# Optimization experiments

Hardware: AMD Instinct MI355X
Metric: run time of the kernel (lower is better)

Reference implementation:

```python
import jax, jax.numpy as jnp
import numpy as np

B, L, C = 64, 4096, 16
PL, PC, NP, D, FS = 128, 8, 64, 64, 100  # patch_size_L, patch_size_C, num_patches, output_dim, f_s


def setup_inputs() -> dict:
    key = jax.random.key(0)
    ks = jax.random.split(key, 9)
    x = jax.random.normal(ks[0], (B, L, C), dtype=jnp.float32)
    start_L = jax.random.randint(ks[1], (B, NP), 0, L - PL + 1, dtype=jnp.int32)
    idx_C = jax.random.randint(ks[2], (B, NP, PC), 0, C, dtype=jnp.int32)
    W1 = jax.random.normal(ks[3], (2 * PC + 1, D), dtype=jnp.float32) * 0.2
    b1 = jax.random.normal(ks[4], (D,), dtype=jnp.float32) * 0.02
    W2 = jax.random.normal(ks[5], (2 * D + 1, D), dtype=jnp.float32) * 0.1
    b2 = jax.random.normal(ks[6], (D,), dtype=jnp.float32) * 0.02
    W3 = jax.random.normal(ks[7], (PL * D, D), dtype=jnp.float32) * 0.01
    b3 = jax.random.normal(ks[8], (D,), dtype=jnp.float32) * 0.02
    return dict(x=x, start_L=start_L, idx_C=idx_C, W1=W1, b1=b1, W2=W2, b2=b2, W3=W3, b3=b3)


def reference(x, start_L, idx_C, W1, b1, W2, b2, W3, b3):
    T = 1.0 / FS
    # contiguous window indices along L (wrapped), [B, NP, PL]
    idx_L = (start_L[:, :, None] + jnp.arange(PL, dtype=jnp.int32)) % L
    # fused double gather: avoid materializing the [B, NP, L, C] broadcast of the original
    bidx = jnp.arange(B)[:, None, None, None]
    patches = x[bidx, idx_L[:, :, :, None], idx_C[:, :, None, :]]        # [B, NP, PL, PC]
    # time embedding: t = arange(L)*T gathered by idx_L
    t_patches = (idx_L.astype(jnp.float32) * T)[..., None]               # [B, NP, PL, 1]
    # channel embedding: c = arange(C) gathered by idx_C
    c_patches = jnp.broadcast_to(idx_C.astype(jnp.float32)[:, :, None, :], (B, NP, PL, PC))
    feats = jnp.concatenate([patches, t_patches, c_patches], axis=-1)    # [B, NP, PL, 2*PC+1]
    h = jax.nn.silu(feats @ W1 + b1)                                     # [B, NP, PL, D]
    # --- fft branch (computed then discarded by the original module; kept for fidelity) ---
    f = jnp.linspace(0.0, FS / 2.0, PL // 2 + 1)
    fft = jnp.fft.rfft(h, axis=-2, norm='ortho')                         # [B, NP, PL//2+1, D]
    f_patches = jnp.broadcast_to(f[None, None, :, None], (B, NP, PL // 2 + 1, 1))
    fcat = jnp.concatenate([fft.real, fft.imag, f_patches], axis=-1)     # [B, NP, PL//2+1, 2D+1]
    _unused = jax.nn.silu(fcat @ W2 + b2)
    # --- mixer on flattened patches ---
    flat = h.reshape(B, NP, PL * D)                                      # [B, NP, PL*D]
    out = jax.nn.silu(flat @ W3 + b3)                                    # [B, NP, D]
    return out
```

## Files before the change

kernel.cpp:

```cpp
#include <hip/hip_runtime.h>
#include <hip/hip_bf16.h>

#define BB 64
#define LL 4096
#define CC 16
#define PL 128
#define PC 8
#define NPP 64
#define DD 64
#define TSTEP 0.01f

#define KSPLIT 16
#define LT_PER (PL / KSPLIT)
#define NT_MAIN 256
#define NMB BB

#define FRAG_U32 (PL * 8 * 256)
#define SPLIT_STRIDE (NMB * 2 * 2 * 64 * 16)
#define PART_FLT (KSPLIT * SPLIT_STRIDE)

typedef float f32x4  __attribute__((ext_vector_type(4)));
typedef float f32x16 __attribute__((ext_vector_type(16)));
typedef int   i32x4  __attribute__((ext_vector_type(4)));
typedef short s16x8  __attribute__((ext_vector_type(8)));
typedef unsigned int u32;

__device__ __forceinline__ u32 f2bf(float f) {
    u32 u = __float_as_uint(f);
    return (u + 0x7fffu + ((u >> 16) & 1u)) >> 16;
}
__device__ __forceinline__ float silu_f(float z) {
    return z * __builtin_amdgcn_rcpf(1.0f + __expf(-z));
}
__device__ __forceinline__ u32 pk(float lo, float hi) {
    __hip_bfloat162 p = __float22bfloat162_rn(float2{lo, hi});
    u32 r;
    __builtin_memcpy(&r, &p, 4);
    return r;
}
__device__ __forceinline__ s16x8 as8(i32x4 v) {
    s16x8 r;
    __builtin_memcpy(&r, &v, 16);
    return r;
}
__device__ __forceinline__ void plswap(u32& a, u32& b) {
    auto r = __builtin_amdgcn_permlane32_swap(a, b, false, false);
    u32 tmp[2];
    __builtin_memcpy(tmp, &r, 8);
    a = tmp[0]; b = tmp[1];
}

__global__ __launch_bounds__(256) void w3_prep(const float* __restrict__ W3,
                                               u32* __restrict__ wsf) {
    const int tid  = blockIdx.x * 256 + threadIdx.x;
    const int lane = tid & 63;
    const int m    = tid >> 6;
    const int ns   = m & 1;
    const int ksub = (m >> 1) & 1;
    const int kk   = (m >> 2) & 1;
    const int ltg  = m >> 3;
    const int k0   = ltg * 64 + kk * 32 + ksub * 16 + ((lane >> 5) << 3);
    const int col  = (ns << 5) + (lane & 31);
    u32 q[4];
    #pragma unroll
    for (int jj = 0; jj < 4; ++jj)
        q[jj] = pk(W3[(size_t)(k0 + 2 * jj)     * DD + col],
                   W3[(size_t)(k0 + 2 * jj + 1) * DD + col]);
    i32x4 v; v.x = (int)q[0]; v.y = (int)q[1]; v.z = (int)q[2]; v.w = (int)q[3];
    *(i32x4*)(wsf + (size_t)m * 256 + (lane << 2)) = v;
}

__global__ __launch_bounds__(NT_MAIN) void htfe_main(
    const float* __restrict__ x, const int* __restrict__ start_L,
    const int* __restrict__ idx_C, const float* __restrict__ W1,
    const float* __restrict__ b1, const u32* __restrict__ wsf,
    float* __restrict__ part)
{
    __shared__ __align__(16) u32    xqf[LT_PER * 64 * 8];
    __shared__ __align__(16) f32x16 redacc[2][2][64];
    __shared__ int sStart[64];
    __shared__ int sCi[64][PC];

    const int t    = threadIdx.x;
    const int lane = t & 63;
    const int w    = t >> 6;
    const int kk   = w >> 1;
    const int ph   = w & 1;
    const int l31  = lane & 31;
    const bool loH = lane < 32;

    const int mb    = blockIdx.x & (NMB - 1);
    const int split = blockIdx.x >> 6;
    const int b     = mb;
    const int lt0   = split * LT_PER;

    if (t < 64) sStart[t] = start_L[b * NPP + t];
    {
        const int i0 = t, i1 = t + 256;
        sCi[i0 >> 3][i0 & 7] = idx_C[(size_t)b * NPP * PC + i0];
        sCi[i1 >> 3][i1 & 7] = idx_C[(size_t)b * NPP * PC + i1];
    }
    __syncthreads();

    const int p  = ph * 32 + l31;
    const int dA = kk * 32 + l31;
    const float startPf = (float)sStart[p];

    i32x4 a1f0, a1f1;
    if (loH) {
        a1f0.x = (int)pk(W1[0 * DD + dA], W1[1 * DD + dA]);
        a1f0.y = (int)pk(W1[2 * DD + dA], W1[3 * DD + dA]);
        a1f0.z = (int)pk(W1[4 * DD + dA], W1[5 * DD + dA]);
        a1f0.w = (int)pk(W1[6 * DD + dA], W1[7 * DD + dA]);
        a1f1.x = (int)pk(W1[8 * DD + dA], W1[8 * DD + dA]);
        a1f1.y = (int)pk(b1[dA], 0.0f);
        a1f1.z = 0; a1f1.w = 0;
    } else {
        a1f0.x = (int)pk(W1[ 9 * DD + dA], W1[10 * DD + dA]);
        a1f0.y = (int)pk(W1[11 * DD + dA], W1[12 * DD + dA]);
        a1f0.z = (int)pk(W1[13 * DD + dA], W1[14 * DD + dA]);
        a1f0.w = (int)pk(W1[15 * DD + dA], W1[16 * DD + dA]);
        a1f1.x = (int)pk(W1[0 * DD + dA], W1[1 * DD + dA]);
        a1f1.y = (int)pk(W1[2 * DD + dA], W1[3 * DD + dA]);
        a1f1.z = (int)pk(W1[4 * DD + dA], W1[5 * DD + dA]);
        a1f1.w = (int)pk(W1[6 * DD + dA], W1[7 * DD + dA]);
    }
    i32x4 cReg;
    cReg.x = (int)pk((float)sCi[p][0], (float)sCi[p][1]);
    cReg.y = (int)pk((float)sCi[p][2], (float)sCi[p][3]);
    cReg.z = (int)pk((float)sCi[p][4], (float)sCi[p][5]);
    cReg.w = (int)pk((float)sCi[p][6], (float)sCi[p][7]);

    #pragma unroll
    for (int uu = 0; uu < 2; ++uu) {
        const int u  = t * 2 + uu;
        const int lt = u >> 6;
        const int pp = u & 63;
        const float* xrow = x + ((size_t)b * LL + (size_t)(sStart[pp] + lt0 + lt)) * CC;
        u32 qh[4], ql[4];
        #pragma unroll
        for (int c2 = 0; c2 < 4; ++c2) {
            const float v0 = xrow[sCi[pp][2 * c2]];
            const float v1 = xrow[sCi[pp][2 * c2 + 1]];
            const u32 h0 = f2bf(v0), h1 = f2bf(v1);
            qh[c2] = h0 | (h1 << 16);
            ql[c2] = f2bf(v0 - __uint_as_float(h0 << 16)) |
                     (f2bf(v1 - __uint_as_float(h1 << 16)) << 16);
        }
        const int swz = ((pp >> 2) & 1) << 2;
        u32* dst = xqf + lt * 512 + pp * 8;
        i32x4 vh; vh.x=(int)qh[0]; vh.y=(int)qh[1]; vh.z=(int)qh[2]; vh.w=(int)qh[3];
        i32x4 vl; vl.x=(int)ql[0]; vl.y=(int)ql[1]; vl.z=(int)ql[2]; vl.w=(int)ql[3];
        *(i32x4*)(dst + (0 ^ swz)) = vh;
        *(i32x4*)(dst + (4 ^ swz)) = vl;
    }
    __syncthreads();

    f32x16 acc0 = {}, acc1 = {};
    const u32* bsrc = wsf + ((size_t)lt0 * 8 + (size_t)kk * 4) * 256 + (lane << 2);
    const u32 ONEP = pk(1.0f, 0.0f);
    const u32* xrd = xqf + p * 8 + ((((lane >> 5) << 2) ^ (((p >> 2) & 1) << 2)));

    #pragma unroll 2
    for (int lt = 0; lt < LT_PER; ++lt) {
        const i32x4 bf00 = *(const i32x4*)(bsrc);
        const i32x4 bf01 = *(const i32x4*)(bsrc + 256);
        const i32x4 bf10 = *(const i32x4*)(bsrc + 512);
        const i32x4 bf11 = *(const i32x4*)(bsrc + 768);
        bsrc += 2048;

        const i32x4 rd = *(const i32x4*)(xrd + lt * 512);

        const float tf  = (startPf + (float)(lt0 + lt)) * TSTEP;
        const u32   tb  = f2bf(tf);
        const u32   tpk2 = tb | (f2bf(tf - __uint_as_float(tb << 16)) << 16);
        i32x4 tvec; tvec.x = (int)tpk2; tvec.y = (int)ONEP; tvec.z = 0; tvec.w = 0;

        const i32x4 b0f = loH ? rd : cReg;
        const i32x4 b1f = loH ? tvec : rd;

        f32x16 hp = {};
        hp = __builtin_amdgcn_mfma_f32_32x32x16_bf16(as8(a1f0), as8(b0f), hp, 0, 0, 0);
        hp = __builtin_amdgcn_mfma_f32_32x32x16_bf16(as8(a1f1), as8(b1f), hp, 0, 0, 0);

        u32 P[8];
        #pragma unroll
        for (int j = 0; j < 8; ++j)
            P[j] = pk(silu_f(hp[2 * j]), silu_f(hp[2 * j + 1]));

        plswap(P[0], P[2]); plswap(P[1], P[3]);
        plswap(P[4], P[6]); plswap(P[5], P[7]);
        i32x4 af0; af0.x=(int)P[0]; af0.y=(int)P[1]; af0.z=(int)P[2]; af0.w=(int)P[3];
        i32x4 af1; af1.x=(int)P[4]; af1.y=(int)P[5]; af1.z=(int)P[6]; af1.w=(int)P[7];

        acc0 = __builtin_amdgcn_mfma_f32_32x32x16_bf16(as8(af0), as8(bf00), acc0, 0, 0, 0);
        acc0 = __builtin_amdgcn_mfma_f32_32x32x16_bf16(as8(af1), as8(bf10), acc0, 0, 0, 0);
        acc1 = __builtin_amdgcn_mfma_f32_32x32x16_bf16(as8(af0), as8(bf01), acc1, 0, 0, 0);
        acc1 = __builtin_amdgcn_mfma_f32_32x32x16_bf16(as8(af1), as8(bf11), acc1, 0, 0, 0);
    }

    if (kk == 1) {
        redacc[ph][0][lane] = acc0;
        redacc[ph][1][lane] = acc1;
    }
    __syncthreads();
    if (kk == 0) {
        const f32x16 r0 = redacc[ph][0][lane];
        const f32x16 r1 = redacc[ph][1][lane];
        float* pd0 = part + ((((size_t)split * NMB + mb) * 2 + ph) * 2 + 0) * 1024 + (lane << 4);
        float* pd1 = pd0 + 1024;
        #pragma unroll
        for (int q = 0; q < 4; ++q) {
            f32x4 o0, o1;
            #pragma unroll
            for (int j = 0; j < 4; ++j) {
                o0[j] = acc0[q * 4 + j] + r0[q * 4 + j];
                o1[j] = acc1[q * 4 + j] + r1[q * 4 + j];
            }
            *(f32x4*)(pd0 + q * 4) = o0;
            *(f32x4*)(pd1 + q * 4) = o1;
        }
    }
}

__global__ __launch_bounds__(256) void finish_reduce(const float* __restrict__ part,
                                                     const float* __restrict__ b3,
                                                     float* __restrict__ out) {
    const int tid  = blockIdx.x * 256 + threadIdx.x;
    const int rq   = tid & 3;
    const int lane = (tid >> 2) & 63;
    const int ns   = (tid >> 8) & 1;
    const int ph   = (tid >> 9) & 1;
    const int mb   = tid >> 10;
    const int l31  = lane & 31;
    const float* src = part + (((size_t)mb * 2 + ph) * 2 + ns) * 1024 + (lane << 4) + (rq << 2);
    f32x4 s = {0.f, 0.f, 0.f, 0.f};
    #pragma unroll
    for (int sp = 0; sp < KSPLIT; ++sp) {
        const f32x4 v = *(const f32x4*)(src + (size_t)sp * SPLIT_STRIDE);
        s.x += v.x; s.y += v.y; s.z += v.z; s.w += v.w;
    }
    const int col  = (ns << 5) + l31;
    const float bias = b3[col];
    #pragma unroll
    for (int j = 0; j < 4; ++j) {
        const int prow = ph * 32 + j + 8 * rq + 4 * (lane >> 5);
        out[((size_t)mb * NPP + prow) * DD + col] = silu_f(s[j] + bias);
    }
}

extern "C" void kernel_launch(void* const* d_in, const int* in_sizes, int n_in,
                              void* d_out, int out_size, void* d_ws, size_t ws_size,
                              hipStream_t stream) {
    const float* x       = (const float*)d_in[0];
    const int*   start_L = (const int*)  d_in[1];
    const int*   idx_C   = (const int*)  d_in[2];
    const float* W1      = (const float*)d_in[3];
    const float* b1      = (const float*)d_in[4];
    const float* W3      = (const float*)d_in[7];
    const float* b3      = (const float*)d_in[8];
    float* out  = (float*)d_out;
    u32*   wsf  = (u32*)d_ws;
    float* part = (float*)(wsf + FRAG_U32);

    w3_prep<<<256, 256, 0, stream>>>(W3, wsf);
    htfe_main<<<NMB * KSPLIT, NT_MAIN, 0, stream>>>(x, start_L, idx_C, W1, b1, wsf, part);
    finish_reduce<<<256, 256, 0, stream>>>(part, b3, out);
}
```

Before: 38.30 us.

## Stage x rows via coalesced vector loads into LDS before channel gather

Replaces the per-element scattered global gather of x with coalesced float4 loads of whole 16-channel rows into a padded shared-memory arena. The channel selection then reads from LDS. The xqf layout changes to separate hi/lo planes instead of a swizzled interleave, and the reduction buffer reuses the arena. The finish_reduce block index mapping is also permuted. This adds two extra barrier passes and loads all 16 channels instead of 8, but aims to cut uncoalesced global traffic.

```diff
diff --git a/kernel.cpp b/kernel.cpp
--- a/kernel.cpp
+++ b/kernel.cpp
@@ -76,8 +76,8 @@
     const float* __restrict__ b1, const u32* __restrict__ wsf,
     float* __restrict__ part)
 {
-    __shared__ __align__(16) u32    xqf[LT_PER * 64 * 8];
-    __shared__ __align__(16) f32x16 redacc[2][2][64];
+    __shared__ __align__(64) float arena[256 * 17];
+    __shared__ __align__(16) u32   xqf[LT_PER * 512];
     __shared__ int sStart[64];
     __shared__ int sCi[64][PC];
 
@@ -100,7 +100,47 @@
         sCi[i0 >> 3][i0 & 7] = idx_C[(size_t)b * NPP * PC + i0];
         sCi[i1 >> 3][i1 & 7] = idx_C[(size_t)b * NPP * PC + i1];
     }
+    const int pGat = t & 63;
+    const i32x4 ciA = *(const i32x4*)(idx_C + (size_t)b * NPP * PC + pGat * 8);
+    const i32x4 ciB = *(const i32x4*)(idx_C + (size_t)b * NPP * PC + pGat * 8 + 4);
     __syncthreads();
+
+    #pragma unroll
+    for (int pass = 0; pass < 2; ++pass) {
+        #pragma unroll
+        for (int q = 0; q < 4; ++q) {
+            const int i    = q * 256 + t;
+            const int row  = i >> 2;
+            const int quad = i & 3;
+            const int pp   = row & 63;
+            const int gRow = sStart[pp] + lt0 + pass * 4 + (row >> 6);
+            const f32x4 v = *(const f32x4*)(x + ((size_t)b * LL + (size_t)gRow) * CC + quad * 4);
+            *(f32x4*)(arena + row * 17 + quad * 4) = v;
+        }
+        __syncthreads();
+        {
+            const float* rb = arena + t * 17;
+            int cis[8];
+            cis[0]=ciA.x; cis[1]=ciA.y; cis[2]=ciA.z; cis[3]=ciA.w;
+            cis[4]=ciB.x; cis[5]=ciB.y; cis[6]=ciB.z; cis[7]=ciB.w;
+            u32 qh[4], ql[4];
+            #pragma unroll
+            for (int c2 = 0; c2 < 4; ++c2) {
+                const float v0 = rb[cis[2 * c2]];
+                const float v1 = rb[cis[2 * c2 + 1]];
+                const u32 h0 = f2bf(v0), h1 = f2bf(v1);
+                qh[c2] = h0 | (h1 << 16);
+                ql[c2] = f2bf(v0 - __uint_as_float(h0 << 16)) |
+                         (f2bf(v1 - __uint_as_float(h1 << 16)) << 16);
+            }
+            u32* dst = xqf + (pass * 4 + (t >> 6)) * 512 + pGat * 4;
+            i32x4 vh; vh.x=(int)qh[0]; vh.y=(int)qh[1]; vh.z=(int)qh[2]; vh.w=(int)qh[3];
+            i32x4 vl; vl.x=(int)ql[0]; vl.y=(int)ql[1]; vl.z=(int)ql[2]; vl.w=(int)ql[3];
+            *(i32x4*)(dst)       = vh;
+            *(i32x4*)(dst + 256) = vl;
+        }
+        __syncthreads();
+    }
 
     const int p  = ph * 32 + l31;
     const int dA = kk * 32 + l31;
@@ -131,35 +171,10 @@
     cReg.z = (int)pk((float)sCi[p][4], (float)sCi[p][5]);
     cReg.w = (int)pk((float)sCi[p][6], (float)sCi[p][7]);
 
-    #pragma unroll
-    for (int uu = 0; uu < 2; ++uu) {
-        const int u  = t * 2 + uu;
-        const int lt = u >> 6;
-        const int pp = u & 63;
-        const float* xrow = x + ((size_t)b * LL + (size_t)(sStart[pp] + lt0 + lt)) * CC;
-        u32 qh[4], ql[4];
-        #pragma unroll
-        for (int c2 = 0; c2 < 4; ++c2) {
-            const float v0 = xrow[sCi[pp][2 * c2]];
-            const float v1 = xrow[sCi[pp][2 * c2 + 1]];
-            const u32 h0 = f2bf(v0), h1 = f2bf(v1);
-            qh[c2] = h0 | (h1 << 16);
-            ql[c2] = f2bf(v0 - __uint_as_float(h0 << 16)) |
-                     (f2bf(v1 - __uint_as_float(h1 << 16)) << 16);
-        }
-        const int swz = ((pp >> 2) & 1) << 2;
-        u32* dst = xqf + lt * 512 + pp * 8;
-        i32x4 vh; vh.x=(int)qh[0]; vh.y=(int)qh[1]; vh.z=(int)qh[2]; vh.w=(int)qh[3];
-        i32x4 vl; vl.x=(int)ql[0]; vl.y=(int)ql[1]; vl.z=(int)ql[2]; vl.w=(int)ql[3];
-        *(i32x4*)(dst + (0 ^ swz)) = vh;
-        *(i32x4*)(dst + (4 ^ swz)) = vl;
-    }
-    __syncthreads();
-
     f32x16 acc0 = {}, acc1 = {};
     const u32* bsrc = wsf + ((size_t)lt0 * 8 + (size_t)kk * 4) * 256 + (lane << 2);
     const u32 ONEP = pk(1.0f, 0.0f);
-    const u32* xrd = xqf + p * 8 + ((((lane >> 5) << 2) ^ (((p >> 2) & 1) << 2)));
+    const u32* xrd = xqf + ((lane >> 5) << 8) + (p << 2);
 
     #pragma unroll 2
     for (int lt = 0; lt < LT_PER; ++lt) {
@@ -199,14 +214,16 @@
         acc1 = __builtin_amdgcn_mfma_f32_32x32x16_bf16(as8(af1), as8(bf11), acc1, 0, 0, 0);
     }
 
+    f32x16* redacc = (f32x16*)arena;
+    __syncthreads();
     if (kk == 1) {
-        redacc[ph][0][lane] = acc0;
-        redacc[ph][1][lane] = acc1;
+        redacc[(ph * 2 + 0) * 64 + lane] = acc0;
+        redacc[(ph * 2 + 1) * 64 + lane] = acc1;
     }
     __syncthreads();
     if (kk == 0) {
-        const f32x16 r0 = redacc[ph][0][lane];
-        const f32x16 r1 = redacc[ph][1][lane];
+        const f32x16 r0 = redacc[(ph * 2 + 0) * 64 + lane];
+        const f32x16 r1 = redacc[(ph * 2 + 1) * 64 + lane];
         float* pd0 = part + ((((size_t)split * NMB + mb) * 2 + ph) * 2 + 0) * 1024 + (lane << 4);
         float* pd1 = pd0 + 1024;
         #pragma unroll
@@ -226,12 +243,14 @@
 __global__ __launch_bounds__(256) void finish_reduce(const float* __restrict__ part,
                                                      const float* __restrict__ b3,
                                                      float* __restrict__ out) {
-    const int tid  = blockIdx.x * 256 + threadIdx.x;
-    const int rq   = tid & 3;
-    const int lane = (tid >> 2) & 63;
-    const int ns   = (tid >> 8) & 1;
-    const int ph   = (tid >> 9) & 1;
-    const int mb   = tid >> 10;
+    const int bid   = blockIdx.x;
+    const int mb    = bid & 63;
+    const int chunk = bid >> 6;
+    const int idx10 = chunk * 256 + threadIdx.x;
+    const int rq   = idx10 & 3;
+    const int lane = (idx10 >> 2) & 63;
+    const int ns   = (idx10 >> 8) & 1;
+    const int ph   = (idx10 >> 9) & 1;
     const int l31  = lane & 31;
     const float* src = part + (((size_t)mb * 2 + ph) * 2 + ns) * 1024 + (lane << 4) + (rq << 2);
     f32x4 s = {0.f, 0.f, 0.f, 0.f};
```

Measured after the change: 36.37 us. 5.1% less time.
